# Performance work log

Measured on AMD Instinct MI355X. Metric: run time of the kernel, lower is better.

The kernel has to match this reference:

```python
import jax, jax.numpy as jnp
import numpy as np

N, E = 50000, 400000
IN, HID, LAT = 64, 64, 64


def _lin(key, fi, fo):
    return jax.random.normal(key, (fi, fo), jnp.float32) / np.sqrt(fi)


def setup_inputs() -> dict:
    key = jax.random.key(0)
    ks = jax.random.split(key, 24)
    inp = {
        'x': jax.random.normal(ks[0], (N, IN), jnp.float32),
        'edge_index': jax.random.randint(ks[1], (2, E), 0, N, dtype=jnp.int32),
        'batch': jnp.zeros((N,), jnp.int32),
    }
    # conv1: heads=1, out=HID, no residual
    inp.update(Wl1=_lin(ks[2], IN, HID), bl1=jnp.zeros(HID), Wr1=_lin(ks[3], IN, HID), br1=jnp.zeros(HID),
               att1=jax.random.normal(ks[4], (1, HID)) / np.sqrt(HID), bo1=jnp.zeros(HID))
    # conv2: heads=4, out=2*HID//4 per head (concat -> 2*HID), residual
    O2 = 2 * HID // 4
    inp.update(Wl2=_lin(ks[5], HID, 4 * O2), bl2=jnp.zeros(4 * O2), Wr2=_lin(ks[6], HID, 4 * O2), br2=jnp.zeros(4 * O2),
               att2=jax.random.normal(ks[7], (4, O2)) / np.sqrt(O2), bo2=jnp.zeros(4 * O2), Wres2=_lin(ks[8], HID, 4 * O2))
    # conv3: heads=4, out=HID per head (concat -> 4*HID), residual
    O3 = HID
    inp.update(Wl3=_lin(ks[9], 2 * HID, 4 * O3), bl3=jnp.zeros(4 * O3), Wr3=_lin(ks[10], 2 * HID, 4 * O3), br3=jnp.zeros(4 * O3),
               att3=jax.random.normal(ks[11], (4, O3)) / np.sqrt(O3), bo3=jnp.zeros(4 * O3), Wres3=_lin(ks[12], 2 * HID, 4 * O3))
    inp.update(ln1_g=jnp.ones(HID), ln1_b=jnp.zeros(HID), ln2_g=jnp.ones(2 * HID), ln2_b=jnp.zeros(2 * HID),
               ln3_g=jnp.ones(4 * HID), ln3_b=jnp.zeros(4 * HID))
    inp.update(enc_W=_lin(ks[13], 4 * HID, LAT), enc_b=jnp.zeros(LAT), rp_W=_lin(ks[14], IN, LAT), rp_b=jnp.zeros(LAT))
    inp.update(d1_W=_lin(ks[15], LAT, 2 * HID), d1_b=jnp.zeros(2 * HID), d2_W=_lin(ks[16], 2 * HID, HID), d2_b=jnp.zeros(HID),
               d3_W=_lin(ks[17], HID, IN), d3_b=jnp.zeros(IN))
    return inp


def _gatv2(x, src, tgt, Wl, bl, Wr, br, att, bo, heads, oc, Wres=None):
    # GATv2: e_ij = att . leaky_relu(Wr x_i + Wl x_j), softmax over in-neighbors of i,
    # out_i = sum_j alpha_ij * (Wl x_j); concat heads; optional linear residual.
    n = x.shape[0]
    xl = (x @ Wl + bl).reshape(n, heads, oc)  # source transform
    xr = (x @ Wr + br).reshape(n, heads, oc)  # target transform
    xj = xl[src]                              # [E, H, C] gathered source feats
    e = jnp.einsum('ehc,hc->eh', jax.nn.leaky_relu(xr[tgt] + xj, 0.2), att)
    m = jax.ops.segment_max(e, tgt, num_segments=n)          # stable segment softmax
    p = jnp.exp(e - m[tgt])
    alpha = p / jax.ops.segment_sum(p, tgt, num_segments=n)[tgt]
    out = jax.ops.segment_sum(alpha[:, :, None] * xj, tgt, num_segments=n).reshape(n, heads * oc)
    if Wres is not None:
        out = out + x @ Wres
    return out + bo


def _gnorm(x, g, b):
    # PyG LayerNorm(mode='graph') with batch=None: normalize over ALL nodes and features
    mu = jnp.mean(x)
    d = x - mu
    var = jnp.mean(d * d)
    return d * jax.lax.rsqrt(var + 1e-5) * g + b


def reference(x, edge_index, batch, Wl1, bl1, Wr1, br1, att1, bo1,
              Wl2, bl2, Wr2, br2, att2, bo2, Wres2,
              Wl3, bl3, Wr3, br3, att3, bo3, Wres3,
              ln1_g, ln1_b, ln2_g, ln2_b, ln3_g, ln3_b,
              enc_W, enc_b, rp_W, rp_b, d1_W, d1_b, d2_W, d2_b, d3_W, d3_b):
    n = x.shape[0]
    loop = jnp.arange(n, dtype=edge_index.dtype)  # add_self_loops=True (GATv2Conv default)
    src = jnp.concatenate([edge_index[0], loop])
    tgt = jnp.concatenate([edge_index[1], loop])
    h1 = jax.nn.relu(_gnorm(_gatv2(x, src, tgt, Wl1, bl1, Wr1, br1, att1, bo1, 1, HID), ln1_g, ln1_b))
    h2 = jax.nn.relu(_gnorm(_gatv2(h1, src, tgt, Wl2, bl2, Wr2, br2, att2, bo2, 4, 2 * HID // 4, Wres2), ln2_g, ln2_b))
    h3 = jax.nn.relu(_gnorm(_gatv2(h2, src, tgt, Wl3, bl3, Wr3, br3, att3, bo3, 4, HID, Wres3), ln3_g, ln3_b))
    z_nodes = jax.nn.relu(h3 @ enc_W + enc_b) + (x @ rp_W + rp_b)  # dropout inactive (eval)
    ones = jnp.ones((n, 1), z_nodes.dtype)
    z_graph = jax.ops.segment_sum(z_nodes, batch, num_segments=1) / jax.ops.segment_sum(ones, batch, num_segments=1)
    h = jax.nn.relu(z_nodes @ d1_W + d1_b)
    h = jax.nn.relu(h @ d2_W + d2_b)
    x_hat = h @ d3_W + d3_b
    return (z_nodes, x_hat, z_graph)
```

## Files before the change

### kernel.cpp

```cpp
#include <hip/hip_runtime.h>
#include <math.h>

typedef __attribute__((ext_vector_type(8))) short short8;
typedef __attribute__((ext_vector_type(4))) float f32x4;

__device__ __forceinline__ unsigned short f2bf(float f) {
  union { float f; unsigned u; } c; c.f = f;
  unsigned r = c.u + 0x7fffu + ((c.u >> 16) & 1u);
  return (unsigned short)(r >> 16);
}
__device__ __forceinline__ float bf2f(unsigned short u) {
  union { unsigned u; float f; } c; c.u = ((unsigned)u) << 16;
  return c.f;
}

__global__ void zero_k(int* __restrict__ deg, int n, float* __restrict__ stats,
                       float* __restrict__ zg) {
  int i = blockIdx.x * 256 + threadIdx.x;
  if (i < n) deg[i] = 0;
  if (i < 768) stats[i] = 0.f;
  if (i < 64) zg[i] = 0.f;
}

__global__ void hist_k(const int* __restrict__ tgt, int* __restrict__ deg, int E) {
  int stride = gridDim.x * blockDim.x;
  for (int e = blockIdx.x * blockDim.x + threadIdx.x; e < E; e += stride)
    atomicAdd(&deg[tgt[e]], 1);
}

__global__ void scan1_k(const int* __restrict__ deg, int* __restrict__ bsum, int n) {
  __shared__ int sh[256];
  int idx = blockIdx.x * 256 + threadIdx.x;
  sh[threadIdx.x] = (idx < n) ? deg[idx] : 0;
  __syncthreads();
  for (int off = 128; off > 0; off >>= 1) {
    if (threadIdx.x < off) sh[threadIdx.x] += sh[threadIdx.x + off];
    __syncthreads();
  }
  if (threadIdx.x == 0) bsum[blockIdx.x] = sh[0];
}

__global__ void scan2_k(int* __restrict__ bsum, int nb) {
  __shared__ int sh[256];
  int t = threadIdx.x;
  int v = (t < nb) ? bsum[t] : 0;
  sh[t] = v; __syncthreads();
  for (int off = 1; off < 256; off <<= 1) {
    int add = (t >= off) ? sh[t - off] : 0;
    __syncthreads();
    sh[t] += add;
    __syncthreads();
  }
  if (t < nb) bsum[t] = sh[t] - v;
}

__global__ void scan3_k(const int* __restrict__ deg, const int* __restrict__ bsum,
                        int* __restrict__ starts, int* __restrict__ cursor, int n) {
  __shared__ int sh[256];
  int t = threadIdx.x;
  int idx = blockIdx.x * 256 + t;
  int v = (idx < n) ? deg[idx] : 0;
  sh[t] = v; __syncthreads();
  for (int off = 1; off < 256; off <<= 1) {
    int add = (t >= off) ? sh[t - off] : 0;
    __syncthreads();
    sh[t] += add;
    __syncthreads();
  }
  if (idx < n) {
    int ex = bsum[blockIdx.x] + sh[t] - v;
    starts[idx] = ex;
    cursor[idx] = ex;
  }
}

__global__ void scatter_k(const int* __restrict__ src, const int* __restrict__ tgt,
                          int* __restrict__ cursor, int* __restrict__ esrc, int E) {
  int stride = gridDim.x * blockDim.x;
  for (int e = blockIdx.x * blockDim.x + threadIdx.x; e < E; e += stride) {
    int p = atomicAdd(&cursor[tgt[e]], 1);
    esrc[p] = src[e];
  }
}

__global__ void cvt_k(const float* __restrict__ src, unsigned short* __restrict__ dst,
                      size_t n4) {
  size_t stride = (size_t)gridDim.x * blockDim.x;
  for (size_t i = (size_t)blockIdx.x * blockDim.x + threadIdx.x; i < n4; i += stride) {
    float4 v = reinterpret_cast<const float4*>(src)[i];
    ushort4 o;
    o.x = f2bf(v.x); o.y = f2bf(v.y); o.z = f2bf(v.z); o.w = f2bf(v.w);
    reinterpret_cast<ushort4*>(dst)[i] = o;
  }
}

struct WSeg { const float* W; unsigned short* T; int K; int F; int base; };
struct WPack { WSeg s[13]; int total; };
__global__ __launch_bounds__(256) void wconv_all_k(WPack p) {
  int idx = blockIdx.x * 256 + threadIdx.x;
  if (idx >= p.total) return;
  int si = 0;
#pragma unroll
  for (int i = 1; i < 13; ++i) si = (idx >= p.s[i].base) ? i : si;
  const WSeg sg = p.s[si];
  const int loc = idx - sg.base;
  const int k = loc / sg.F, f = loc - k * sg.F;
  sg.T[(size_t)f * sg.K + k] = f2bf(sg.W[loc]);
}

template <int K, int F, int SETS, int LNF, int BF16IN, int ACT1, int W32_1>
__global__ __launch_bounds__(256) void mg_k(
    const void* __restrict__ Xv, const float* __restrict__ bins,
    const float* __restrict__ lng, const float* __restrict__ lnb, float invNF,
    const unsigned short* __restrict__ WT0, const float* __restrict__ B0,
    const unsigned short* __restrict__ WT1, const float* __restrict__ B1,
    const unsigned short* __restrict__ WT2,
    unsigned short* __restrict__ Y0, unsigned short* __restrict__ Y1,
    float* __restrict__ Y2, int n) {
  constexpr int NK = K / 32;
  constexpr int TL = F / 64;
  constexpr int CPR = K / 8;
  __shared__ unsigned short As[64 * K];
  __shared__ float lnp[2];
  char* asb = (char*)As;
  const int tid = threadIdx.x;
  const int lane = tid & 63;
  const int wv = tid >> 6;
  const int r0 = blockIdx.x * 64;

  if (LNF) {
    if (tid < 64) {
      float s1 = bins[tid] + bins[tid + 64];
      float s2 = bins[tid + 128] + bins[tid + 192];
#pragma unroll
      for (int mm = 1; mm < 64; mm <<= 1) {
        s1 += __shfl_xor(s1, mm, 64);
        s2 += __shfl_xor(s2, mm, 64);
      }
      if (tid == 0) {
        const float mu = s1 * invNF;
        lnp[0] = mu;
        lnp[1] = rsqrtf(s2 * invNF - mu * mu + 1e-5f);
      }
    }
    __syncthreads();
  }
  const float mu = LNF ? lnp[0] : 0.f;
  const float rs = LNF ? lnp[1] : 0.f;

  for (int c = tid; c < 64 * CPR; c += 256) {
    const int row = c / CPR;
    const int k0 = (c - row * CPR) * 8;
    const int gr = r0 + row;
    short8 a = {0, 0, 0, 0, 0, 0, 0, 0};
    if (gr < n) {
      if (BF16IN) {
        a = *reinterpret_cast<const short8*>((const unsigned short*)Xv +
                                             (size_t)gr * K + k0);
      } else {
        const float* Xf = (const float*)Xv + (size_t)gr * K + k0;
        float v[8];
        *(float4*)&v[0] = *(const float4*)&Xf[0];
        *(float4*)&v[4] = *(const float4*)&Xf[4];
        if (LNF) {
          float g[8], bb[8];
          *(float4*)&g[0] = *(const float4*)&lng[k0];
          *(float4*)&g[4] = *(const float4*)&lng[k0 + 4];
          *(float4*)&bb[0] = *(const float4*)&lnb[k0];
          *(float4*)&bb[4] = *(const float4*)&lnb[k0 + 4];
#pragma unroll
          for (int q = 0; q < 8; ++q)
            v[q] = fmaxf(fmaf(v[q] - mu, rs * g[q], bb[q]), 0.f);
        }
#pragma unroll
        for (int q = 0; q < 8; ++q) a[q] = (short)f2bf(v[q]);
      }
    }
    const int boff = ((row * K + k0) * 2) ^ ((row & 7) << 4);
    *(short8*)(asb + boff) = a;
  }
  __syncthreads();

  const int rl = lane & 15;
  const int ks = lane >> 4;
#pragma unroll
  for (int set = 0; set < SETS; ++set) {
    const unsigned short* WT = (set == 0) ? WT0 : (set == 1) ? WT1 : WT2;
    f32x4 acc[4][TL];
#pragma unroll
    for (int rt = 0; rt < 4; ++rt)
#pragma unroll
      for (int t = 0; t < TL; ++t) acc[rt][t] = (f32x4){0.f, 0.f, 0.f, 0.f};
#pragma unroll
    for (int kk = 0; kk < NK; ++kk) {
      short8 bf[TL];
#pragma unroll
      for (int t = 0; t < TL; ++t)
        bf[t] = *reinterpret_cast<const short8*>(
            &WT[(size_t)((wv * TL + t) * 16 + rl) * K + kk * 32 + ks * 8]);
      short8 af[4];
#pragma unroll
      for (int rt = 0; rt < 4; ++rt) {
        const int row = rt * 16 + rl;
        const int boff = ((row * K + kk * 32 + ks * 8) * 2) ^ ((row & 7) << 4);
        af[rt] = *(const short8*)(asb + boff);
      }
#pragma unroll
      for (int rt = 0; rt < 4; ++rt)
#pragma unroll
        for (int t = 0; t < TL; ++t)
          acc[rt][t] =
              __builtin_amdgcn_mfma_f32_16x16x32_bf16(af[rt], bf[t], acc[rt][t], 0, 0, 0);
    }
#pragma unroll
    for (int rt = 0; rt < 4; ++rt) {
      const int rowd = r0 + rt * 16 + ks * 4;
#pragma unroll
      for (int t = 0; t < TL; ++t) {
        const int col = (wv * TL + t) * 16 + rl;
        const float bias = (set == 0) ? B0[col] : (set == 1) ? B1[col] : 0.f;
#pragma unroll
        for (int r = 0; r < 4; ++r) {
          const int gr = rowd + r;
          if (gr >= n) continue;
          float o = acc[rt][t][r] + bias;
          const size_t idx = (size_t)gr * F + col;
          if (set == 0) {
            if (ACT1) o = fmaxf(o, 0.f);
            if (W32_1) Y2[idx] = o; else Y0[idx] = f2bf(o);
          } else if (set == 1) {
            Y1[idx] = f2bf(o);
          } else {
            Y2[idx] = o;
          }
        }
      }
    }
  }
}

__global__ __launch_bounds__(256) void enc_k(
    const float* __restrict__ h3, const float* __restrict__ bins,
    const float* __restrict__ lng, const float* __restrict__ lnb, float invNF,
    const unsigned short* __restrict__ WTe, const float* __restrict__ Be,
    const unsigned short* __restrict__ xb, const unsigned short* __restrict__ WTrp,
    const float* __restrict__ Brp, float* __restrict__ z,
    unsigned short* __restrict__ zb, int n) {
  constexpr int K1 = 256, K2 = 64, F = 64;
  __shared__ unsigned short As1[64 * K1];
  __shared__ unsigned short As2[64 * K2];
  __shared__ float lnp[2];
  char* a1b = (char*)As1;
  char* a2b = (char*)As2;
  const int tid = threadIdx.x;
  const int lane = tid & 63;
  const int wv = tid >> 6;
  const int r0 = blockIdx.x * 64;

  if (tid < 64) {
    float s1 = bins[tid] + bins[tid + 64];
    float s2 = bins[tid + 128] + bins[tid + 192];
#pragma unroll
    for (int mm = 1; mm < 64; mm <<= 1) {
      s1 += __shfl_xor(s1, mm, 64);
      s2 += __shfl_xor(s2, mm, 64);
    }
    if (tid == 0) {
      const float mu = s1 * invNF;
      lnp[0] = mu;
      lnp[1] = rsqrtf(s2 * invNF - mu * mu + 1e-5f);
    }
  }
  __syncthreads();
  const float mu = lnp[0], rs = lnp[1];

  for (int c = tid; c < 64 * (K1 / 8); c += 256) {
    const int row = c / (K1 / 8);
    const int k0 = (c - row * (K1 / 8)) * 8;
    const int gr = r0 + row;
    short8 a = {0, 0, 0, 0, 0, 0, 0, 0};
    if (gr < n) {
      const float* Xf = h3 + (size_t)gr * K1 + k0;
      float v[8], g[8], bb[8];
      *(float4*)&v[0] = *(const float4*)&Xf[0];
      *(float4*)&v[4] = *(const float4*)&Xf[4];
      *(float4*)&g[0] = *(const float4*)&lng[k0];
      *(float4*)&g[4] = *(const float4*)&lng[k0 + 4];
      *(float4*)&bb[0] = *(const float4*)&lnb[k0];
      *(float4*)&bb[4] = *(const float4*)&lnb[k0 + 4];
#pragma unroll
      for (int q = 0; q < 8; ++q) {
        float t = fmaxf(fmaf(v[q] - mu, rs * g[q], bb[q]), 0.f);
        a[q] = (short)f2bf(t);
      }
    }
    const int boff = ((row * K1 + k0) * 2) ^ ((row & 7) << 4);
    *(short8*)(a1b + boff) = a;
  }
  for (int c = tid; c < 64 * (K2 / 8); c += 256) {
    const int row = c / (K2 / 8);
    const int k0 = (c - row * (K2 / 8)) * 8;
    const int gr = r0 + row;
    short8 a = {0, 0, 0, 0, 0, 0, 0, 0};
    if (gr < n)
      a = *reinterpret_cast<const short8*>(&xb[(size_t)gr * K2 + k0]);
    const int boff = ((row * K2 + k0) * 2) ^ ((row & 7) << 4);
    *(short8*)(a2b + boff) = a;
  }
  __syncthreads();

  const int rl = lane & 15;
  const int ks = lane >> 4;
  f32x4 a1[4], a2[4];
#pragma unroll
  for (int rt = 0; rt < 4; ++rt) {
    a1[rt] = (f32x4){0.f, 0.f, 0.f, 0.f};
    a2[rt] = (f32x4){0.f, 0.f, 0.f, 0.f};
  }
#pragma unroll
  for (int kk = 0; kk < K1 / 32; ++kk) {
    short8 bf = *reinterpret_cast<const short8*>(
        &WTe[(size_t)(wv * 16 + rl) * K1 + kk * 32 + ks * 8]);
#pragma unroll
    for (int rt = 0; rt < 4; ++rt) {
      const int row = rt * 16 + rl;
      const int boff = ((row * K1 + kk * 32 + ks * 8) * 2) ^ ((row & 7) << 4);
      short8 af = *(const short8*)(a1b + boff);
      a1[rt] = __builtin_amdgcn_mfma_f32_16x16x32_bf16(af, bf, a1[rt], 0, 0, 0);
    }
  }
#pragma unroll
  for (int kk = 0; kk < K2 / 32; ++kk) {
    short8 bf = *reinterpret_cast<const short8*>(
        &WTrp[(size_t)(wv * 16 + rl) * K2 + kk * 32 + ks * 8]);
#pragma unroll
    for (int rt = 0; rt < 4; ++rt) {
      const int row = rt * 16 + rl;
      const int boff = ((row * K2 + kk * 32 + ks * 8) * 2) ^ ((row & 7) << 4);
      short8 af = *(const short8*)(a2b + boff);
      a2[rt] = __builtin_amdgcn_mfma_f32_16x16x32_bf16(af, bf, a2[rt], 0, 0, 0);
    }
  }
  const int col = wv * 16 + rl;
  const float be = Be[col];
  const float brp = Brp[col];
#pragma unroll
  for (int rt = 0; rt < 4; ++rt) {
    const int rowd = r0 + rt * 16 + ks * 4;
#pragma unroll
    for (int r = 0; r < 4; ++r) {
      const int gr = rowd + r;
      if (gr >= n) continue;
      const float o = fmaxf(a1[rt][r] + be, 0.f) + a2[rt][r] + brp;
      const size_t idx = (size_t)gr * F + col;
      z[idx] = o;
      zb[idx] = f2bf(o);
    }
  }
}

template <int VEC> struct RawT;
template <> struct RawT<1> { using T = unsigned short; };
template <> struct RawT<2> { using T = unsigned; };
template <> struct RawT<4> { using T = unsigned long long; };

__device__ __forceinline__ void bdec(unsigned short u, float* o) { o[0] = bf2f(u); }
__device__ __forceinline__ void bdec(unsigned u, float* o) {
  o[0] = bf2f((unsigned short)(u & 0xffffu));
  o[1] = bf2f((unsigned short)(u >> 16));
}
__device__ __forceinline__ void bdec(unsigned long long u, float* o) {
  o[0] = bf2f((unsigned short)(u & 0xffffu));
  o[1] = bf2f((unsigned short)((u >> 16) & 0xffffu));
  o[2] = bf2f((unsigned short)((u >> 32) & 0xffffu));
  o[3] = bf2f((unsigned short)(u >> 48));
}

template <int H, int C, int VEC, int HAS_RES>
__global__ __launch_bounds__(256) void agg_k(
    const unsigned short* __restrict__ xl, const unsigned short* __restrict__ xr,
    const float* __restrict__ att, const float* __restrict__ bo,
    const int* __restrict__ starts, const int* __restrict__ deg,
    const int* __restrict__ esrc, float* __restrict__ out,
    float* __restrict__ bins, int n) {
  constexpr int F = H * C;
  constexpr int G = 64 / H;
  constexpr int CS = F / VEC;
  using RT = typename RawT<VEC>::T;
  const int lane = threadIdx.x & 63;
  const int wv = threadIdx.x >> 6;
  const int node = blockIdx.x * 4 + wv;
  const bool active = node < n;
  float s1w = 0.f, s2w = 0.f;

  if (active) {
    const RT* xlr = reinterpret_cast<const RT*>(xl);
    float xri[VEC], av[VEC], acc[VEC];
    {
      RT rx = reinterpret_cast<const RT*>(xr)[(size_t)node * CS + lane];
      bdec(rx, xri);
    }
#pragma unroll
    for (int q = 0; q < VEC; ++q) {
      av[q] = att[lane * VEC + q];
      acc[q] = 0.f;
    }
    float m = -1e30f, s = 0.f;
    const int st = starts[node];
    const int cnt = deg[node];
    const int total = cnt + 1;
    RT u0, u1 = 0;
    {
      int j0 = (cnt > 0) ? esrc[st] : node;
      u0 = xlr[(size_t)j0 * CS + lane];
    }
    if (total > 1) {
      int j1 = (1 < cnt) ? esrc[st + 1] : node;
      u1 = xlr[(size_t)j1 * CS + lane];
    }
    int it = 0;
    for (; it + 2 <= total; it += 2) {
      RT n0 = u0, n1 = u1;
      if (it + 2 < total) {
        int jn = (it + 2 < cnt) ? esrc[st + it + 2] : node;
        n0 = xlr[(size_t)jn * CS + lane];
      }
      if (it + 3 < total) {
        int jn = (it + 3 < cnt) ? esrc[st + it + 3] : node;
        n1 = xlr[(size_t)jn * CS + lane];
      }
      float x0[VEC], x1[VEC];
      bdec(u0, x0);
      bdec(u1, x1);
      float e0 = 0.f, e1 = 0.f;
#pragma unroll
      for (int q = 0; q < VEC; ++q) {
        float t0 = xri[q] + x0[q];
        float t1 = xri[q] + x1[q];
        t0 = (t0 > 0.f) ? t0 : 0.2f * t0;
        t1 = (t1 > 0.f) ? t1 : 0.2f * t1;
        e0 = fmaf(t0, av[q], e0);
        e1 = fmaf(t1, av[q], e1);
      }
#pragma unroll
      for (int mask = 1; mask < G; mask <<= 1) {
        e0 += __shfl_xor(e0, mask, 64);
        e1 += __shfl_xor(e1, mask, 64);
      }
      const float eM = fmaxf(e0, e1);
      if (eM - m > 8.f) {
        const float sc = __expf(m - eM);
        s *= sc;
#pragma unroll
        for (int q = 0; q < VEC; ++q) acc[q] *= sc;
        m = eM;
      }
      const float p0 = __expf(e0 - m);
      const float p1 = __expf(e1 - m);
      s += p0 + p1;
#pragma unroll
      for (int q = 0; q < VEC; ++q)
        acc[q] = fmaf(p0, x0[q], fmaf(p1, x1[q], acc[q]));
      u0 = n0;
      u1 = n1;
    }
    if (it < total) {
      float x0[VEC];
      bdec(u0, x0);
      float e0 = 0.f;
#pragma unroll
      for (int q = 0; q < VEC; ++q) {
        float t0 = xri[q] + x0[q];
        t0 = (t0 > 0.f) ? t0 : 0.2f * t0;
        e0 = fmaf(t0, av[q], e0);
      }
#pragma unroll
      for (int mask = 1; mask < G; mask <<= 1) e0 += __shfl_xor(e0, mask, 64);
      if (e0 - m > 8.f) {
        const float sc = __expf(m - e0);
        s *= sc;
#pragma unroll
        for (int q = 0; q < VEC; ++q) acc[q] *= sc;
        m = e0;
      }
      const float p0 = __expf(e0 - m);
      s += p0;
#pragma unroll
      for (int q = 0; q < VEC; ++q) acc[q] = fmaf(p0, x0[q], acc[q]);
    }
    const float inv = 1.f / s;
#pragma unroll
    for (int q = 0; q < VEC; ++q) {
      const size_t idx = (size_t)node * F + lane * VEC + q;
      float o = acc[q] * inv + bo[lane * VEC + q];
      if (HAS_RES) o += out[idx];
      out[idx] = o;
      s1w += o;
      s2w += o * o;
    }
  }
#pragma unroll
  for (int mask = 1; mask < 64; mask <<= 1) {
    s1w += __shfl_xor(s1w, mask, 64);
    s2w += __shfl_xor(s2w, mask, 64);
  }
  __shared__ float sh[8];
  if (lane == 0) { sh[wv] = s1w; sh[4 + wv] = s2w; }
  __syncthreads();
  if (threadIdx.x == 0) {
    const int bin = blockIdx.x & 127;
    atomicAdd(&bins[bin], sh[0] + sh[1] + sh[2] + sh[3]);
    atomicAdd(&bins[128 + bin], sh[4] + sh[5] + sh[6] + sh[7]);
  }
}

__global__ void colmean_k(const float* __restrict__ z, float* __restrict__ outv,
                          int n, float inv) {
  __shared__ float sh[256];
  int col = threadIdx.x & 63;
  int w = threadIdx.x >> 6;
  float s = 0.f;
  for (int r = blockIdx.x * 4 + w; r < n; r += gridDim.x * 4)
    s += z[(size_t)r * 64 + col];
  sh[threadIdx.x] = s;
  __syncthreads();
  if (threadIdx.x < 64) {
    float t = sh[threadIdx.x] + sh[threadIdx.x + 64] + sh[threadIdx.x + 128] +
              sh[threadIdx.x + 192];
    atomicAdd(&outv[col], t * inv);
  }
}

extern "C" void kernel_launch(void* const* d_in, const int* in_sizes, int n_in,
                              void* d_out, int out_size, void* d_ws, size_t ws_size,
                              hipStream_t stream) {
  const float* x = (const float*)d_in[0];
  const int* ei = (const int*)d_in[1];
  const float *Wl1 = (const float*)d_in[3], *bl1 = (const float*)d_in[4];
  const float *Wr1 = (const float*)d_in[5], *br1 = (const float*)d_in[6];
  const float *att1 = (const float*)d_in[7], *bo1 = (const float*)d_in[8];
  const float *Wl2 = (const float*)d_in[9], *bl2 = (const float*)d_in[10];
  const float *Wr2 = (const float*)d_in[11], *br2 = (const float*)d_in[12];
  const float *att2 = (const float*)d_in[13], *bo2 = (const float*)d_in[14];
  const float *Wres2 = (const float*)d_in[15];
  const float *Wl3 = (const float*)d_in[16], *bl3 = (const float*)d_in[17];
  const float *Wr3 = (const float*)d_in[18], *br3 = (const float*)d_in[19];
  const float *att3 = (const float*)d_in[20], *bo3 = (const float*)d_in[21];
  const float *Wres3 = (const float*)d_in[22];
  const float *ln1g = (const float*)d_in[23], *ln1b = (const float*)d_in[24];
  const float *ln2g = (const float*)d_in[25], *ln2b = (const float*)d_in[26];
  const float *ln3g = (const float*)d_in[27], *ln3b = (const float*)d_in[28];
  const float *encW = (const float*)d_in[29], *encb = (const float*)d_in[30];
  const float *rpW = (const float*)d_in[31], *rpb = (const float*)d_in[32];
  const float *d1W = (const float*)d_in[33], *d1b = (const float*)d_in[34];
  const float *d2W = (const float*)d_in[35], *d2b = (const float*)d_in[36];
  const float *d3W = (const float*)d_in[37], *d3b = (const float*)d_in[38];

  const int N = in_sizes[0] / 64;
  const int E = in_sizes[1] / 2;
  const int* esrc_in = ei;
  const int* etgt_in = ei + E;

  char* cur = (char*)d_ws;
  auto take = [&](size_t bytes) {
    char* p = cur;
    cur += (bytes + 15) & ~(size_t)15;
    return p;
  };
  float* bufC = (float*)take((size_t)N * 256 * 4);
  float* bufD = (float*)take((size_t)N * 128 * 4);
  unsigned short* Ab = (unsigned short*)take((size_t)N * 256 * 2);
  unsigned short* Bb = (unsigned short*)take((size_t)N * 256 * 2);
  unsigned short* Cb = (unsigned short*)take((size_t)N * 256 * 2);
  unsigned short* Db = (unsigned short*)take((size_t)N * 128 * 2);
  unsigned short* xb = (unsigned short*)take((size_t)N * 64 * 2);
  float* stats = (float*)take(768 * 4);
  int* deg = (int*)take((size_t)N * 4);
  int* starts = (int*)take((size_t)N * 4);
  int* cursor = (int*)take((size_t)N * 4);
  int* bsum = (int*)take(1024);
  int* esrc = (int*)take((size_t)E * 4);
  auto wt = [&](int K, int F) { return (unsigned short*)take((size_t)K * F * 2); };
  unsigned short *Tl1 = wt(64, 64), *Tr1 = wt(64, 64);
  unsigned short *Tl2 = wt(64, 128), *Tr2 = wt(64, 128), *Tres2 = wt(64, 128);
  unsigned short *Tl3 = wt(128, 256), *Tr3 = wt(128, 256), *Tres3 = wt(128, 256);
  unsigned short *Tenc = wt(256, 64), *Trp = wt(64, 64);
  unsigned short *Td1 = wt(64, 128), *Td2 = wt(128, 64), *Td3 = wt(64, 64);
  if ((size_t)(cur - (char*)d_ws) > ws_size) return;

  float* z = (float*)d_out;
  float* xhat = z + (size_t)N * 64;
  float* zg = xhat + (size_t)N * 64;

  zero_k<<<(N + 255) / 256, 256, 0, stream>>>(deg, N, stats, zg);

  {
    WPack p;
    const float* Ws[13] = {Wl1, Wr1, Wl2, Wr2, Wres2, Wl3, Wr3, Wres3,
                           encW, rpW, d1W, d2W, d3W};
    unsigned short* Ts[13] = {Tl1, Tr1, Tl2, Tr2, Tres2, Tl3, Tr3, Tres3,
                              Tenc, Trp, Td1, Td2, Td3};
    const int Ks[13] = {64, 64, 64, 64, 64, 128, 128, 128, 256, 64, 64, 128, 64};
    const int Fs[13] = {64, 64, 128, 128, 128, 256, 256, 256, 64, 64, 128, 64, 64};
    int base = 0;
    for (int i = 0; i < 13; ++i) {
      p.s[i] = {Ws[i], Ts[i], Ks[i], Fs[i], base};
      base += Ks[i] * Fs[i];
    }
    p.total = base;
    wconv_all_k<<<(base + 255) / 256, 256, 0, stream>>>(p);
  }
  cvt_k<<<1024, 256, 0, stream>>>(x, xb, (size_t)N * 16);

  const int nb = (N + 255) / 256;
  hist_k<<<512, 256, 0, stream>>>(etgt_in, deg, E);
  scan1_k<<<nb, 256, 0, stream>>>(deg, bsum, N);
  scan2_k<<<1, 256, 0, stream>>>(bsum, nb);
  scan3_k<<<nb, 256, 0, stream>>>(deg, bsum, starts, cursor, N);
  scatter_k<<<512, 256, 0, stream>>>(esrc_in, etgt_in, cursor, esrc, E);

  const int gblk = (N + 63) / 64;
  const int ablk = (N + 3) / 4;
  const float* nullf = nullptr;
  unsigned short* nullb = nullptr;
  float* nully = nullptr;

  mg_k<64, 64, 2, 0, 1, 0, 0><<<gblk, 256, 0, stream>>>(
      xb, nullf, nullf, nullf, 0.f, Tl1, bl1, Tr1, br1, nullb, Ab, Bb, nully, N);
  agg_k<1, 64, 1, 0><<<ablk, 256, 0, stream>>>(Ab, Bb, att1, bo1, starts, deg, esrc,
                                               bufC, stats + 0, N);
  mg_k<64, 128, 3, 1, 0, 0, 0><<<gblk, 256, 0, stream>>>(
      bufC, stats + 0, ln1g, ln1b, 1.f / ((float)N * 64.f), Tl2, bl2, Tr2, br2, Tres2,
      Ab, Bb, bufD, N);
  agg_k<4, 32, 2, 1><<<ablk, 256, 0, stream>>>(Ab, Bb, att2, bo2, starts, deg, esrc,
                                               bufD, stats + 256, N);
  mg_k<128, 256, 3, 1, 0, 0, 0><<<gblk, 256, 0, stream>>>(
      bufD, stats + 256, ln2g, ln2b, 1.f / ((float)N * 128.f), Tl3, bl3, Tr3, br3,
      Tres3, Ab, Bb, bufC, N);
  agg_k<4, 64, 4, 1><<<ablk, 256, 0, stream>>>(Ab, Bb, att3, bo3, starts, deg, esrc,
                                               bufC, stats + 512, N);
  enc_k<<<gblk, 256, 0, stream>>>(bufC, stats + 512, ln3g, ln3b,
                                  1.f / ((float)N * 256.f), Tenc, encb, xb, Trp, rpb, z,
                                  xb, N);
  colmean_k<<<256, 256, 0, stream>>>(z, zg, N, 1.f / (float)N);

  mg_k<64, 128, 1, 0, 1, 1, 0><<<gblk, 256, 0, stream>>>(
      xb, nullf, nullf, nullf, 0.f, Td1, d1b, nullb, nullf, nullb, Db, nullb, nully, N);
  mg_k<128, 64, 1, 0, 1, 1, 0><<<gblk, 256, 0, stream>>>(
      Db, nullf, nullf, nullf, 0.f, Td2, d2b, nullb, nullf, nullb, Cb, nullb, nully, N);
  mg_k<64, 64, 1, 0, 1, 0, 1><<<gblk, 256, 0, stream>>>(
      Cb, nullf, nullf, nullf, 0.f, Td3, d3b, nullb, nullf, nullb, nullb, nullb, xhat, N);
}
```

Before: 557.1 us.

## Store GAT features in fp16/bf16 and use packed dot2 attention scoring

```diff
diff --git a/kernel.cpp b/kernel.cpp
--- a/kernel.cpp
+++ b/kernel.cpp
@@ -3,6 +3,7 @@
 
 typedef __attribute__((ext_vector_type(8))) short short8;
 typedef __attribute__((ext_vector_type(4))) float f32x4;
+typedef _Float16 h2 __attribute__((ext_vector_type(2)));
 
 __device__ __forceinline__ unsigned short f2bf(float f) {
   union { float f; unsigned u; } c; c.f = f;
@@ -12,6 +13,9 @@
 __device__ __forceinline__ float bf2f(unsigned short u) {
   union { unsigned u; float f; } c; c.u = ((unsigned)u) << 16;
   return c.f;
+}
+__device__ __forceinline__ void dot2(float& e, h2 a, h2 b) {
+  asm("v_dot2_f32_f16 %0, %1, %2, %0" : "+v"(e) : "v"(a), "v"(b));
 }
 
 __global__ void zero_k(int* __restrict__ deg, int n, float* __restrict__ stats,
@@ -108,15 +112,15 @@
   sg.T[(size_t)f * sg.K + k] = f2bf(sg.W[loc]);
 }
 
-template <int K, int F, int SETS, int LNF, int BF16IN, int ACT1, int W32_1>
+template <int K, int F, int SETS, int LNF, int OM0, int ACT1>
 __global__ __launch_bounds__(256) void mg_k(
-    const void* __restrict__ Xv, const float* __restrict__ bins,
+    const unsigned short* __restrict__ X, const float* __restrict__ bins,
     const float* __restrict__ lng, const float* __restrict__ lnb, float invNF,
     const unsigned short* __restrict__ WT0, const float* __restrict__ B0,
     const unsigned short* __restrict__ WT1, const float* __restrict__ B1,
     const unsigned short* __restrict__ WT2,
-    unsigned short* __restrict__ Y0, unsigned short* __restrict__ Y1,
-    float* __restrict__ Y2, int n) {
+    _Float16* __restrict__ Y0, _Float16* __restrict__ Y1,
+    unsigned short* __restrict__ Y2b, float* __restrict__ Y2f, int n) {
   constexpr int NK = K / 32;
   constexpr int TL = F / 64;
   constexpr int CPR = K / 8;
@@ -154,26 +158,19 @@
     const int gr = r0 + row;
     short8 a = {0, 0, 0, 0, 0, 0, 0, 0};
     if (gr < n) {
-      if (BF16IN) {
-        a = *reinterpret_cast<const short8*>((const unsigned short*)Xv +
-                                             (size_t)gr * K + k0);
-      } else {
-        const float* Xf = (const float*)Xv + (size_t)gr * K + k0;
-        float v[8];
-        *(float4*)&v[0] = *(const float4*)&Xf[0];
-        *(float4*)&v[4] = *(const float4*)&Xf[4];
-        if (LNF) {
-          float g[8], bb[8];
-          *(float4*)&g[0] = *(const float4*)&lng[k0];
-          *(float4*)&g[4] = *(const float4*)&lng[k0 + 4];
-          *(float4*)&bb[0] = *(const float4*)&lnb[k0];
-          *(float4*)&bb[4] = *(const float4*)&lnb[k0 + 4];
-#pragma unroll
-          for (int q = 0; q < 8; ++q)
-            v[q] = fmaxf(fmaf(v[q] - mu, rs * g[q], bb[q]), 0.f);
+      a = *reinterpret_cast<const short8*>(&X[(size_t)gr * K + k0]);
+      if (LNF) {
+        float g[8], bb[8];
+        *(float4*)&g[0] = *(const float4*)&lng[k0];
+        *(float4*)&g[4] = *(const float4*)&lng[k0 + 4];
+        *(float4*)&bb[0] = *(const float4*)&lnb[k0];
+        *(float4*)&bb[4] = *(const float4*)&lnb[k0 + 4];
+#pragma unroll
+        for (int q = 0; q < 8; ++q) {
+          float f = bf2f((unsigned short)a[q]);
+          f = fmaxf(fmaf(f - mu, rs * g[q], bb[q]), 0.f);
+          a[q] = (short)f2bf(f);
         }
-#pragma unroll
-        for (int q = 0; q < 8; ++q) a[q] = (short)f2bf(v[q]);
       }
     }
     const int boff = ((row * K + k0) * 2) ^ ((row & 7) << 4);
@@ -227,11 +224,13 @@
           const size_t idx = (size_t)gr * F + col;
           if (set == 0) {
             if (ACT1) o = fmaxf(o, 0.f);
-            if (W32_1) Y2[idx] = o; else Y0[idx] = f2bf(o);
+            if (OM0 == 0) Y0[idx] = (_Float16)o;
+            else if (OM0 == 1) Y2b[idx] = f2bf(o);
+            else Y2f[idx] = o;
           } else if (set == 1) {
-            Y1[idx] = f2bf(o);
+            Y1[idx] = (_Float16)o;
           } else {
-            Y2[idx] = o;
+            Y2b[idx] = f2bf(o);
           }
         }
       }
@@ -240,7 +239,7 @@
 }
 
 __global__ __launch_bounds__(256) void enc_k(
-    const float* __restrict__ h3, const float* __restrict__ bins,
+    const unsigned short* __restrict__ h3, const float* __restrict__ bins,
     const float* __restrict__ lng, const float* __restrict__ lnb, float invNF,
     const unsigned short* __restrict__ WTe, const float* __restrict__ Be,
     const unsigned short* __restrict__ xb, const unsigned short* __restrict__ WTrp,
@@ -280,18 +279,17 @@
     const int gr = r0 + row;
     short8 a = {0, 0, 0, 0, 0, 0, 0, 0};
     if (gr < n) {
-      const float* Xf = h3 + (size_t)gr * K1 + k0;
-      float v[8], g[8], bb[8];
-      *(float4*)&v[0] = *(const float4*)&Xf[0];
-      *(float4*)&v[4] = *(const float4*)&Xf[4];
+      a = *reinterpret_cast<const short8*>(&h3[(size_t)gr * K1 + k0]);
+      float g[8], bb[8];
       *(float4*)&g[0] = *(const float4*)&lng[k0];
       *(float4*)&g[4] = *(const float4*)&lng[k0 + 4];
       *(float4*)&bb[0] = *(const float4*)&lnb[k0];
       *(float4*)&bb[4] = *(const float4*)&lnb[k0 + 4];
 #pragma unroll
       for (int q = 0; q < 8; ++q) {
-        float t = fmaxf(fmaf(v[q] - mu, rs * g[q], bb[q]), 0.f);
-        a[q] = (short)f2bf(t);
+        float f = bf2f((unsigned short)a[q]);
+        f = fmaxf(fmaf(f - mu, rs * g[q], bb[q]), 0.f);
+        a[q] = (short)f2bf(f);
       }
     }
     const int boff = ((row * K1 + k0) * 2) ^ ((row & 7) << 4);
@@ -302,8 +300,7 @@
     const int k0 = (c - row * (K2 / 8)) * 8;
     const int gr = r0 + row;
     short8 a = {0, 0, 0, 0, 0, 0, 0, 0};
-    if (gr < n)
-      a = *reinterpret_cast<const short8*>(&xb[(size_t)gr * K2 + k0]);
+    if (gr < n) a = *reinterpret_cast<const short8*>(&xb[(size_t)gr * K2 + k0]);
     const int boff = ((row * K2 + k0) * 2) ^ ((row & 7) << 4);
     *(short8*)(a2b + boff) = a;
   }
@@ -360,144 +357,194 @@
 }
 
 template <int VEC> struct RawT;
-template <> struct RawT<1> { using T = unsigned short; };
 template <> struct RawT<2> { using T = unsigned; };
 template <> struct RawT<4> { using T = unsigned long long; };
 
-__device__ __forceinline__ void bdec(unsigned short u, float* o) { o[0] = bf2f(u); }
-__device__ __forceinline__ void bdec(unsigned u, float* o) {
-  o[0] = bf2f((unsigned short)(u & 0xffffu));
-  o[1] = bf2f((unsigned short)(u >> 16));
-}
-__device__ __forceinline__ void bdec(unsigned long long u, float* o) {
-  o[0] = bf2f((unsigned short)(u & 0xffffu));
-  o[1] = bf2f((unsigned short)((u >> 16) & 0xffffu));
-  o[2] = bf2f((unsigned short)((u >> 32) & 0xffffu));
-  o[3] = bf2f((unsigned short)(u >> 48));
-}
-
-template <int H, int C, int VEC, int HAS_RES>
+template <int F, int H, int VEC, int HAS_RES>
 __global__ __launch_bounds__(256) void agg_k(
-    const unsigned short* __restrict__ xl, const unsigned short* __restrict__ xr,
+    const _Float16* __restrict__ xl, const _Float16* __restrict__ xr,
     const float* __restrict__ att, const float* __restrict__ bo,
     const int* __restrict__ starts, const int* __restrict__ deg,
-    const int* __restrict__ esrc, float* __restrict__ out,
+    const int* __restrict__ esrc, unsigned short* __restrict__ out,
     float* __restrict__ bins, int n) {
-  constexpr int F = H * C;
   constexpr int G = 64 / H;
-  constexpr int CS = F / VEC;
+  constexpr int NP = VEC / 2;
   using RT = typename RawT<VEC>::T;
+  union PU { RT r; h2 h[NP]; _Float16 e[VEC]; };
+  const h2 HC = {(_Float16)0.2f, (_Float16)0.2f};
+  const h2 HZ = {(_Float16)0.f, (_Float16)0.f};
   const int lane = threadIdx.x & 63;
   const int wv = threadIdx.x >> 6;
   const int node = blockIdx.x * 4 + wv;
   const bool active = node < n;
+  const int nl = active ? node : 0;
   float s1w = 0.f, s2w = 0.f;
 
+  const RT* xlr = (const RT*)xl;
+  PU xru; xru.r = ((const RT*)xr)[(size_t)nl * 64 + lane];
+  h2 attp[NP];
+  float bov[VEC];
+  PU resu; resu.r = 0;
+#pragma unroll
+  for (int pp = 0; pp < NP; ++pp) {
+    attp[pp][0] = (_Float16)att[lane * VEC + pp * 2];
+    attp[pp][1] = (_Float16)att[lane * VEC + pp * 2 + 1];
+  }
+#pragma unroll
+  for (int q = 0; q < VEC; ++q) bov[q] = bo[lane * VEC + q];
+  unsigned short resb[VEC];
+  if (HAS_RES) {
+#pragma unroll
+    for (int q = 0; q < VEC; ++q) resb[q] = out[(size_t)nl * F + lane * VEC + q];
+  }
+  int st = 0, cnt = 0;
+  if (active) { st = starts[node]; cnt = deg[node]; }
+  const int total = active ? cnt + 1 : 0;
+  auto LD = [&](int i) -> RT {
+    const int j = (i < cnt) ? esrc[st + i] : nl;
+    return xlr[(size_t)j * 64 + lane];
+  };
+  float m = -1e30f, s = 0.f, acc[VEC];
+#pragma unroll
+  for (int q = 0; q < VEC; ++q) acc[q] = 0.f;
+
+  RT q0 = LD(0), q1 = LD(1), q2 = LD(2), q3 = LD(3);
+  for (int it = 0; it < total; it += 2) {
+    const RT f0 = LD(it + 4), f1 = LD(it + 5);
+    PU x0, x1; x0.r = q0; x1.r = q1;
+    float e0 = 0.f, e1 = 0.f;
+#pragma unroll
+    for (int pp = 0; pp < NP; ++pp) {
+      h2 t0 = xru.h[pp] + x0.h[pp];
+      h2 t1 = xru.h[pp] + x1.h[pp];
+      h2 lk0 = __builtin_elementwise_fma(__builtin_elementwise_min(t0, HZ), HC,
+                                         __builtin_elementwise_max(t0, HZ));
+      h2 lk1 = __builtin_elementwise_fma(__builtin_elementwise_min(t1, HZ), HC,
+                                         __builtin_elementwise_max(t1, HZ));
+      dot2(e0, lk0, attp[pp]);
+      dot2(e1, lk1, attp[pp]);
+    }
+#pragma unroll
+    for (int mask = 1; mask < G; mask <<= 1) {
+      e0 += __shfl_xor(e0, mask, 64);
+      e1 += __shfl_xor(e1, mask, 64);
+    }
+    if (it + 1 >= total) e1 = -1e30f;
+    const float eM = fmaxf(e0, e1);
+    if (eM - m > 8.f) {
+      const float sc = __expf(m - eM);
+      s *= sc;
+#pragma unroll
+      for (int q = 0; q < VEC; ++q) acc[q] *= sc;
+      m = eM;
+    }
+    const float p0 = __expf(e0 - m);
+    const float p1 = __expf(e1 - m);
+    s += p0 + p1;
+#pragma unroll
+    for (int q = 0; q < VEC; ++q)
+      acc[q] = fmaf(p0, (float)x0.e[q], fmaf(p1, (float)x1.e[q], acc[q]));
+    q0 = q2; q1 = q3; q2 = f0; q3 = f1;
+  }
   if (active) {
-    const RT* xlr = reinterpret_cast<const RT*>(xl);
-    float xri[VEC], av[VEC], acc[VEC];
-    {
-      RT rx = reinterpret_cast<const RT*>(xr)[(size_t)node * CS + lane];
-      bdec(rx, xri);
-    }
+    const float inv = 1.f / s;
 #pragma unroll
     for (int q = 0; q < VEC; ++q) {
-      av[q] = att[lane * VEC + q];
-      acc[q] = 0.f;
-    }
-    float m = -1e30f, s = 0.f;
-    const int st = starts[node];
-    const int cnt = deg[node];
-    const int total = cnt + 1;
-    RT u0, u1 = 0;
-    {
-      int j0 = (cnt > 0) ? esrc[st] : node;
-      u0 = xlr[(size_t)j0 * CS + lane];
-    }
-    if (total > 1) {
-      int j1 = (1 < cnt) ? esrc[st + 1] : node;
-      u1 = xlr[(size_t)j1 * CS + lane];
-    }
-    int it = 0;
-    for (; it + 2 <= total; it += 2) {
-      RT n0 = u0, n1 = u1;
-      if (it + 2 < total) {
-        int jn = (it + 2 < cnt) ? esrc[st + it + 2] : node;
-        n0 = xlr[(size_t)jn * CS + lane];
-      }
-      if (it + 3 < total) {
-        int jn = (it + 3 < cnt) ? esrc[st + it + 3] : node;
-        n1 = xlr[(size_t)jn * CS + lane];
-      }
-      float x0[VEC], x1[VEC];
-      bdec(u0, x0);
-      bdec(u1, x1);
-      float e0 = 0.f, e1 = 0.f;
-#pragma unroll
-      for (int q = 0; q < VEC; ++q) {
-        float t0 = xri[q] + x0[q];
-        float t1 = xri[q] + x1[q];
-        t0 = (t0 > 0.f) ? t0 : 0.2f * t0;
-        t1 = (t1 > 0.f) ? t1 : 0.2f * t1;
-        e0 = fmaf(t0, av[q], e0);
-        e1 = fmaf(t1, av[q], e1);
-      }
-#pragma unroll
-      for (int mask = 1; mask < G; mask <<= 1) {
-        e0 += __shfl_xor(e0, mask, 64);
-        e1 += __shfl_xor(e1, mask, 64);
-      }
-      const float eM = fmaxf(e0, e1);
-      if (eM - m > 8.f) {
-        const float sc = __expf(m - eM);
-        s *= sc;
-#pragma unroll
-        for (int q = 0; q < VEC; ++q) acc[q] *= sc;
-        m = eM;
-      }
-      const float p0 = __expf(e0 - m);
-      const float p1 = __expf(e1 - m);
-      s += p0 + p1;
-#pragma unroll
-      for (int q = 0; q < VEC; ++q)
-        acc[q] = fmaf(p0, x0[q], fmaf(p1, x1[q], acc[q]));
-      u0 = n0;
-      u1 = n1;
-    }
-    if (it < total) {
-      float x0[VEC];
-      bdec(u0, x0);
-      float e0 = 0.f;
-#pragma unroll
-      for (int q = 0; q < VEC; ++q) {
-        float t0 = xri[q] + x0[q];
-        t0 = (t0 > 0.f) ? t0 : 0.2f * t0;
-        e0 = fmaf(t0, av[q], e0);
-      }
-#pragma unroll
-      for (int mask = 1; mask < G; mask <<= 1) e0 += __shfl_xor(e0, mask, 64);
-      if (e0 - m > 8.f) {
-        const float sc = __expf(m - e0);
-        s *= sc;
-#pragma unroll
-        for (int q = 0; q < VEC; ++q) acc[q] *= sc;
-        m = e0;
-      }
-      const float p0 = __expf(e0 - m);
-      s += p0;
-#pragma unroll
-      for (int q = 0; q < VEC; ++q) acc[q] = fmaf(p0, x0[q], acc[q]);
-    }
-    const float inv = 1.f / s;
-#pragma unroll
-    for (int q = 0; q < VEC; ++q) {
-      const size_t idx = (size_t)node * F + lane * VEC + q;
-      float o = acc[q] * inv + bo[lane * VEC + q];
-      if (HAS_RES) o += out[idx];
-      out[idx] = o;
+      float o = acc[q] * inv + bov[q];
+      if (HAS_RES) o += bf2f(resb[q]);
+      out[(size_t)node * F + lane * VEC + q] = f2bf(o);
       s1w += o;
       s2w += o * o;
     }
+  }
+#pragma unroll
+  for (int mask = 1; mask < 64; mask <<= 1) {
+    s1w += __shfl_xor(s1w, mask, 64);
+    s2w += __shfl_xor(s2w, mask, 64);
+  }
+  __shared__ float sh[8];
+  if (lane == 0) { sh[wv] = s1w; sh[4 + wv] = s2w; }
+  __syncthreads();
+  if (threadIdx.x == 0) {
+    const int bin = blockIdx.x & 127;
+    atomicAdd(&bins[bin], sh[0] + sh[1] + sh[2] + sh[3]);
+    atomicAdd(&bins[128 + bin], sh[4] + sh[5] + sh[6] + sh[7]);
+  }
+}
+
+__global__ __launch_bounds__(256) void agg1_k(
+    const _Float16* __restrict__ xl, const _Float16* __restrict__ xr,
+    const float* __restrict__ att, const float* __restrict__ bo,
+    const int* __restrict__ starts, const int* __restrict__ deg,
+    const int* __restrict__ esrc, unsigned short* __restrict__ out,
+    float* __restrict__ bins, int n) {
+  union PU { unsigned r; h2 h; _Float16 e[2]; };
+  const h2 HC = {(_Float16)0.2f, (_Float16)0.2f};
+  const h2 HZ = {(_Float16)0.f, (_Float16)0.f};
+  const int lane = threadIdx.x & 63;
+  const int wv = threadIdx.x >> 6;
+  const int l32 = lane & 31;
+  const int node = blockIdx.x * 8 + wv * 2 + (lane >> 5);
+  const bool active = node < n;
+  const int nl = active ? node : 0;
+  float s1w = 0.f, s2w = 0.f;
+
+  const unsigned* xlr = (const unsigned*)xl;
+  PU xru; xru.r = ((const unsigned*)xr)[(size_t)nl * 32 + l32];
+  h2 attp = {(_Float16)att[l32 * 2], (_Float16)att[l32 * 2 + 1]};
+  const float bo0 = bo[l32 * 2], bo1 = bo[l32 * 2 + 1];
+  int st = 0, cnt = 0;
+  if (active) { st = starts[node]; cnt = deg[node]; }
+  const int total = active ? cnt + 1 : 0;
+  const int mt = max(total, __shfl_xor(total, 32, 64));
+  auto LD = [&](int i) -> unsigned {
+    const int j = (i < cnt) ? esrc[st + i] : nl;
+    return xlr[(size_t)j * 32 + l32];
+  };
+  float m = -1e30f, s = 0.f, a0 = 0.f, a1 = 0.f;
+  unsigned q0 = LD(0), q1 = LD(1), q2 = LD(2), q3 = LD(3);
+  for (int it = 0; it < mt; it += 2) {
+    const unsigned f0 = LD(it + 4), f1 = LD(it + 5);
+    PU x0, x1; x0.r = q0; x1.r = q1;
+    float e0 = 0.f, e1 = 0.f;
+    {
+      h2 t0 = xru.h + x0.h;
+      h2 t1 = xru.h + x1.h;
+      h2 lk0 = __builtin_elementwise_fma(__builtin_elementwise_min(t0, HZ), HC,
+                                         __builtin_elementwise_max(t0, HZ));
+      h2 lk1 = __builtin_elementwise_fma(__builtin_elementwise_min(t1, HZ), HC,
+                                         __builtin_elementwise_max(t1, HZ));
+      dot2(e0, lk0, attp);
+      dot2(e1, lk1, attp);
+    }
+#pragma unroll
+    for (int mask = 1; mask < 32; mask <<= 1) {
+      e0 += __shfl_xor(e0, mask, 64);
+      e1 += __shfl_xor(e1, mask, 64);
+    }
+    if (it >= total) e0 = -1e30f;
+    if (it + 1 >= total) e1 = -1e30f;
+    const float eM = fmaxf(e0, e1);
+    if (eM - m > 8.f && eM > -1e29f) {
+      const float sc = __expf(m - eM);
+      s *= sc; a0 *= sc; a1 *= sc;
+      m = eM;
+    }
+    const float p0 = __expf(e0 - m);
+    const float p1 = __expf(e1 - m);
+    s += p0 + p1;
+    a0 = fmaf(p0, (float)x0.e[0], fmaf(p1, (float)x1.e[0], a0));
+    a1 = fmaf(p0, (float)x0.e[1], fmaf(p1, (float)x1.e[1], a1));
+    q0 = q2; q1 = q3; q2 = f0; q3 = f1;
+  }
+  if (active) {
+    const float inv = 1.f / s;
+    const float o0 = a0 * inv + bo0;
+    const float o1 = a1 * inv + bo1;
+    out[(size_t)node * 64 + l32 * 2] = f2bf(o0);
+    out[(size_t)node * 64 + l32 * 2 + 1] = f2bf(o1);
+    s1w = o0 + o1;
+    s2w = o0 * o0 + o1 * o1;
   }
 #pragma unroll
   for (int mask = 1; mask < 64; mask <<= 1) {
@@ -567,10 +614,10 @@
     cur += (bytes + 15) & ~(size_t)15;
     return p;
   };
-  float* bufC = (float*)take((size_t)N * 256 * 4);
-  float* bufD = (float*)take((size_t)N * 128 * 4);
-  unsigned short* Ab = (unsigned short*)take((size_t)N * 256 * 2);
-  unsigned short* Bb = (unsigned short*)take((size_t)N * 256 * 2);
+  unsigned short* bufCb = (unsigned short*)take((size_t)N * 256 * 2);
+  unsigned short* bufDb = (unsigned short*)take((size_t)N * 128 * 2);
+  _Float16* Ab = (_Float16*)take((size_t)N * 256 * 2);
+  _Float16* Bb = (_Float16*)take((size_t)N * 256 * 2);
   unsigned short* Cb = (unsigned short*)take((size_t)N * 256 * 2);
   unsigned short* Db = (unsigned short*)take((size_t)N * 128 * 2);
   unsigned short* xb = (unsigned short*)take((size_t)N * 64 * 2);
@@ -622,32 +669,36 @@
   const int gblk = (N + 63) / 64;
   const int ablk = (N + 3) / 4;
   const float* nullf = nullptr;
+  _Float16* nullh = nullptr;
   unsigned short* nullb = nullptr;
   float* nully = nullptr;
 
-  mg_k<64, 64, 2, 0, 1, 0, 0><<<gblk, 256, 0, stream>>>(
-      xb, nullf, nullf, nullf, 0.f, Tl1, bl1, Tr1, br1, nullb, Ab, Bb, nully, N);
-  agg_k<1, 64, 1, 0><<<ablk, 256, 0, stream>>>(Ab, Bb, att1, bo1, starts, deg, esrc,
-                                               bufC, stats + 0, N);
-  mg_k<64, 128, 3, 1, 0, 0, 0><<<gblk, 256, 0, stream>>>(
-      bufC, stats + 0, ln1g, ln1b, 1.f / ((float)N * 64.f), Tl2, bl2, Tr2, br2, Tres2,
-      Ab, Bb, bufD, N);
-  agg_k<4, 32, 2, 1><<<ablk, 256, 0, stream>>>(Ab, Bb, att2, bo2, starts, deg, esrc,
-                                               bufD, stats + 256, N);
-  mg_k<128, 256, 3, 1, 0, 0, 0><<<gblk, 256, 0, stream>>>(
-      bufD, stats + 256, ln2g, ln2b, 1.f / ((float)N * 128.f), Tl3, bl3, Tr3, br3,
-      Tres3, Ab, Bb, bufC, N);
-  agg_k<4, 64, 4, 1><<<ablk, 256, 0, stream>>>(Ab, Bb, att3, bo3, starts, deg, esrc,
-                                               bufC, stats + 512, N);
-  enc_k<<<gblk, 256, 0, stream>>>(bufC, stats + 512, ln3g, ln3b,
+  mg_k<64, 64, 2, 0, 0, 0><<<gblk, 256, 0, stream>>>(
+      xb, nullf, nullf, nullf, 0.f, Tl1, bl1, Tr1, br1, nullb, Ab, Bb, nullb, nully, N);
+  agg1_k<<<(N + 7) / 8, 256, 0, stream>>>(Ab, Bb, att1, bo1, starts, deg, esrc, bufCb,
+                                          stats + 0, N);
+  mg_k<64, 128, 3, 1, 0, 0><<<gblk, 256, 0, stream>>>(
+      bufCb, stats + 0, ln1g, ln1b, 1.f / ((float)N * 64.f), Tl2, bl2, Tr2, br2, Tres2,
+      Ab, Bb, bufDb, nully, N);
+  agg_k<128, 4, 2, 1><<<ablk, 256, 0, stream>>>(Ab, Bb, att2, bo2, starts, deg, esrc,
+                                                bufDb, stats + 256, N);
+  mg_k<128, 256, 3, 1, 0, 0><<<gblk, 256, 0, stream>>>(
+      bufDb, stats + 256, ln2g, ln2b, 1.f / ((float)N * 128.f), Tl3, bl3, Tr3, br3,
+      Tres3, Ab, Bb, bufCb, nully, N);
+  agg_k<256, 4, 4, 1><<<ablk, 256, 0, stream>>>(Ab, Bb, att3, bo3, starts, deg, esrc,
+                                                bufCb, stats + 512, N);
+  enc_k<<<gblk, 256, 0, stream>>>(bufCb, stats + 512, ln3g, ln3b,
                                   1.f / ((float)N * 256.f), Tenc, encb, xb, Trp, rpb, z,
                                   xb, N);
   colmean_k<<<256, 256, 0, stream>>>(z, zg, N, 1.f / (float)N);
 
-  mg_k<64, 128, 1, 0, 1, 1, 0><<<gblk, 256, 0, stream>>>(
-      xb, nullf, nullf, nullf, 0.f, Td1, d1b, nullb, nullf, nullb, Db, nullb, nully, N);
-  mg_k<128, 64, 1, 0, 1, 1, 0><<<gblk, 256, 0, stream>>>(
-      Db, nullf, nullf, nullf, 0.f, Td2, d2b, nullb, nullf, nullb, Cb, nullb, nully, N);
-  mg_k<64, 64, 1, 0, 1, 0, 1><<<gblk, 256, 0, stream>>>(
-      Cb, nullf, nullf, nullf, 0.f, Td3, d3b, nullb, nullf, nullb, nullb, nullb, xhat, N);
-}
+  mg_k<64, 128, 1, 0, 1, 1><<<gblk, 256, 0, stream>>>(
+      xb, nullf, nullf, nullf, 0.f, Td1, d1b, nullb, nullf, nullb, nullh, nullh, Db,
+      nully, N);
+  mg_k<128, 64, 1, 0, 1, 1><<<gblk, 256, 0, stream>>>(
+      Db, nullf, nullf, nullf, 0.f, Td2, d2b, nullb, nullf, nullb, nullh, nullh, Cb,
+      nully, N);
+  mg_k<64, 64, 1, 0, 2, 0><<<gblk, 256, 0, stream>>>(
+      Cb, nullf, nullf, nullf, 0.f, Td3, d3b, nullb, nullf, nullb, nullh, nullh, nullb,
+      xhat, N);
+}
```

New measurement: 506.9 us. -9.0%, faster.
